# Kernel optimization log

Hardware: AMD Instinct MI355X
Metric: run time of the kernel (lower is better)

The kernel has to match this reference:

```python
import jax, jax.numpy as jnp
import numpy as np

D = 1024
H = 16

def setup_inputs() -> dict:
    key = jax.random.key(0)
    k1, k2, k3 = jax.random.split(key, 3)
    B, T = 4, 2048
    x = jax.random.normal(k1, (B, T, D), dtype=jnp.float32)
    # Linear weights stored as [in, out] so y = x @ W (equivalent to torch Linear with weight.T)
    W_attn = jax.random.normal(k2, (D, 3 * D), dtype=jnp.float32) * (1.0 / np.sqrt(D))
    W_proj = jax.random.normal(k3, (D, D), dtype=jnp.float32) * (1.0 / np.sqrt(D))
    return {"x": x, "W_attn": W_attn, "W_proj": W_proj}

def reference(x, W_attn, W_proj):
    B, T, _ = x.shape
    hd = D // H  # head dim
    qkv = x @ W_attn  # [B,T,3D]
    q, k, v = jnp.split(qkv, 3, axis=-1)
    # [B,T,D] -> [B,H,T,hd]
    q = q.reshape(B, T, H, hd).transpose(0, 2, 1, 3)
    k = k.reshape(B, T, H, hd).transpose(0, 2, 1, 3)
    v = v.reshape(B, T, H, hd).transpose(0, 2, 1, 3)
    scale = 1.0 / np.sqrt(hd).astype(np.float32)
    att = jnp.einsum('bhqd,bhkd->bhqk', q, k) * scale  # [B,H,T,T]
    causal = jnp.tril(jnp.ones((T, T), dtype=bool))
    att = jnp.where(causal[None, None], att, jnp.finfo(att.dtype).min)
    att = jax.nn.softmax(att, axis=-1)
    y = jnp.einsum('bhqk,bhkd->bhqd', att, v)  # [B,H,T,hd]
    y = y.transpose(0, 2, 1, 3).reshape(B, T, D)
    return y @ W_proj
```

## Files before the change

kernel.cpp:

```cpp
#include <hip/hip_runtime.h>


typedef __bf16 bf16;
typedef __attribute__((ext_vector_type(8))) __bf16 bf16x8;
typedef __attribute__((ext_vector_type(4))) __bf16 bf16x4;
typedef __attribute__((ext_vector_type(4))) float f4;

#define BK 32

__device__ __forceinline__ void stage16(const bf16* g, bf16* l) {
    __builtin_amdgcn_global_load_lds((const __attribute__((address_space(1))) void*)g,
                                     (__attribute__((address_space(3))) void*)l,
                                     16, 0, 0);
}

__global__ __launch_bounds__(256)
void cast_f32_bf16(const float* __restrict__ src, bf16* __restrict__ dst, int n4)
{
    int i = blockIdx.x * 256 + threadIdx.x;
    if (i < n4) {
        float4 v = ((const float4*)src)[i];
        bf16x4 o = { (bf16)v.x, (bf16)v.y, (bf16)v.z, (bf16)v.w };
        *(bf16x4*)&dst[i * 4] = o;
    }
}

__global__ __launch_bounds__(256)
void transpose_f32_bf16(const float* __restrict__ src, bf16* __restrict__ dst,
                        int R, int C)
{
    __shared__ bf16 tile[64][65];
    int c0 = blockIdx.x * 64, r0 = blockIdx.y * 64;
    int tid = threadIdx.x;
    for (int i = tid; i < 64 * 64; i += 256) {
        int r = i >> 6, c = i & 63;
        tile[r][c] = (bf16)src[(long)(r0 + r) * C + c0 + c];
    }
    __syncthreads();
    for (int i = tid; i < 64 * 64; i += 256) {
        int r = i >> 6, c = i & 63;
        dst[(long)(c0 + r) * R + r0 + c] = tile[c][r];
    }
}

template <typename OutT>
__global__ __launch_bounds__(256)
void gemm_bt(const bf16* __restrict__ A, const bf16* __restrict__ Bt,
             OutT* __restrict__ C, int M, int N, int K, int lda, int ldc)
{
    __shared__ bf16 As[128 * BK];
    __shared__ bf16 Bs[128 * BK];
    int tid = threadIdx.x;
    int lane = tid & 63;
    int wid = tid >> 6;
    int wy = wid >> 1, wx = wid & 1;

    int nwg = gridDim.x * gridDim.y;
    int bid = blockIdx.y * gridDim.x + blockIdx.x;
    int swz = (bid & 7) * (nwg >> 3) + (bid >> 3);
    int bx = swz % gridDim.x, by = swz / gridDim.x;
    int m0 = by * 128, n0 = bx * 128;

    f4 acc[4][4];
    #pragma unroll
    for (int mi = 0; mi < 4; ++mi)
        #pragma unroll
        for (int ni = 0; ni < 4; ++ni)
            acc[mi][ni] = (f4){0.f, 0.f, 0.f, 0.f};

    int srow = lane >> 2;
    int scol = (lane & 3) * 8;
    for (int kt = 0; kt < K; kt += BK) {
        #pragma unroll
        for (int i = 0; i < 2; ++i) {
            int chunk = wid * 2 + i;
            int row = chunk * 16 + srow;
            stage16(A  + (long)(m0 + row) * lda + kt + scol, As + chunk * 512 + lane * 8);
            stage16(Bt + (long)(n0 + row) * K   + kt + scol, Bs + chunk * 512 + lane * 8);
        }
        __syncthreads();
        bf16x8 af[4], bfr[4];
        #pragma unroll
        for (int mi = 0; mi < 4; ++mi)
            af[mi] = *(const bf16x8*)&As[(wy * 64 + mi * 16 + (lane & 15)) * BK + (lane >> 4) * 8];
        #pragma unroll
        for (int ni = 0; ni < 4; ++ni)
            bfr[ni] = *(const bf16x8*)&Bs[(wx * 64 + ni * 16 + (lane & 15)) * BK + (lane >> 4) * 8];
        #pragma unroll
        for (int mi = 0; mi < 4; ++mi)
            #pragma unroll
            for (int ni = 0; ni < 4; ++ni)
                acc[mi][ni] = __builtin_amdgcn_mfma_f32_16x16x32_bf16(af[mi], bfr[ni], acc[mi][ni], 0, 0, 0);
        __syncthreads();
    }
    #pragma unroll
    for (int mi = 0; mi < 4; ++mi) {
        int rbase = m0 + wy * 64 + mi * 16 + (lane >> 4) * 4;
        #pragma unroll
        for (int ni = 0; ni < 4; ++ni) {
            int col = n0 + wx * 64 + ni * 16 + (lane & 15);
            #pragma unroll
            for (int r = 0; r < 4; ++r)
                C[(long)(rbase + r) * ldc + col] = (OutT)acc[mi][ni][r];
        }
    }
}

#define QS 72
#define C_SL 0.18033688011112042f

__device__ __forceinline__ int vsw(int d, int k) {
    return d * 64 + ((((k >> 3) ^ (d & 7) ^ ((d >> 3) & 7)) & 7) << 3) + (k & 7);
}

__global__ __launch_bounds__(256)
void attn_mfma(bf16* __restrict__ qkv)
{
    __shared__ bf16 Ks[64 * QS];
    __shared__ bf16 Vt[64 * 64];
    __shared__ bf16 Ps[4 * 32 * QS];
    const int T = 2048, D3 = 3072;
    int tid = threadIdx.x;
    int lane = tid & 63, wid = tid >> 6;
    int quad = lane >> 4, col = lane & 15;
    int bh = blockIdx.x & 63;
    int g = blockIdx.x >> 6;
    int qt = ((g >> 2) & 1) ? ((g + 4) & 15) : (15 - g);
    int b = bh >> 4, h = bh & 15;
    long base = (long)b * T * D3 + h * 64;
    int q0 = qt * 128;
    int nk = 2 * qt + 2;
    int srow = tid >> 2, dseg = (tid & 3) * 16;
    bf16* Pw = &Ps[wid * 32 * QS];

    bf16x8 aq[2][2];
    #pragma unroll
    for (int nt = 0; nt < 2; ++nt) {
        const bf16* gq = &qkv[base + (long)(q0 + wid * 32 + nt * 16 + col) * D3 + quad * 8];
        aq[nt][0] = *(const bf16x8*)gq;
        aq[nt][1] = *(const bf16x8*)(gq + 32);
    }
    bf16 one1 = (bf16)1.0f;
    bf16x8 bones = {one1, one1, one1, one1, one1, one1, one1, one1};

    f4 of[2][4], lac[2];
    #pragma unroll
    for (int mg = 0; mg < 2; ++mg) {
        lac[mg] = (f4){0.f, 0.f, 0.f, 0.f};
        #pragma unroll
        for (int n = 0; n < 4; ++n) of[mg][n] = (f4){0.f, 0.f, 0.f, 0.f};
    }

    const bf16* g0 = &qkv[base + (long)srow * D3 + 1024 + dseg];
    bf16x8 kr0 = *(const bf16x8*)g0;
    bf16x8 kr1 = *(const bf16x8*)(g0 + 8);
    bf16x8 vr0 = *(const bf16x8*)(g0 + 1024);
    bf16x8 vr1 = *(const bf16x8*)(g0 + 1032);

    for (int kt = 0; kt < nk; ++kt) {
        __syncthreads();
        *(bf16x8*)&Ks[srow * QS + dseg]     = kr0;
        *(bf16x8*)&Ks[srow * QS + dseg + 8] = kr1;
        #pragma unroll
        for (int j = 0; j < 8; ++j) {
            Vt[vsw(dseg + j, srow)]     = vr0[j];
            Vt[vsw(dseg + 8 + j, srow)] = vr1[j];
        }
        if (kt + 1 < nk) {
            const bf16* gn = &qkv[base + (long)((kt + 1) * 64 + srow) * D3 + 1024 + dseg];
            kr0 = *(const bf16x8*)gn;
            kr1 = *(const bf16x8*)(gn + 8);
            vr0 = *(const bf16x8*)(gn + 1024);
            vr1 = *(const bf16x8*)(gn + 1032);
        }
        __syncthreads();
        bool diag = (kt >= nk - 2);
        int k0 = kt * 64;
        #pragma unroll
        for (int mt = 0; mt < 4; ++mt) {
            bf16x8 ak0 = *(const bf16x8*)&Ks[(mt * 16 + col) * QS + quad * 8];
            bf16x8 ak1 = *(const bf16x8*)&Ks[(mt * 16 + col) * QS + 32 + quad * 8];
            #pragma unroll
            for (int nt = 0; nt < 2; ++nt) {
                f4 z = (f4){0.f, 0.f, 0.f, 0.f};
                __builtin_amdgcn_s_setprio(1);
                z = __builtin_amdgcn_mfma_f32_16x16x32_bf16(ak0, aq[nt][0], z, 0, 0, 0);
                f4 st = __builtin_amdgcn_mfma_f32_16x16x32_bf16(ak1, aq[nt][1], z, 0, 0, 0);
                __builtin_amdgcn_s_setprio(0);
                bf16x4 pk;
                if (diag) {
                    int qg = q0 + wid * 32 + nt * 16 + col;
                    #pragma unroll
                    for (int r = 0; r < 4; ++r) {
                        float arg = fmaf(st[r], C_SL, -16.f);
                        if ((k0 + mt * 16 + quad * 4 + r) > qg) arg = -1e30f;
                        pk[r] = (bf16)exp2f(arg);
                    }
                } else {
                    #pragma unroll
                    for (int r = 0; r < 4; ++r)
                        pk[r] = (bf16)exp2f(fmaf(st[r], C_SL, -16.f));
                }
                *(bf16x4*)&Pw[(nt * 16 + col) * QS + mt * 16 + quad * 4] = pk;
            }
        }
        bf16x8 ap[2][2];
        #pragma unroll
        for (int mg = 0; mg < 2; ++mg) {
            ap[mg][0] = *(const bf16x8*)&Pw[(mg * 16 + col) * QS + quad * 8];
            ap[mg][1] = *(const bf16x8*)&Pw[(mg * 16 + col) * QS + 32 + quad * 8];
        }
        #pragma unroll
        for (int nd = 0; nd < 4; ++nd) {
            bf16x8 bv0 = *(const bf16x8*)&Vt[vsw(nd * 16 + col, quad * 8)];
            bf16x8 bv1 = *(const bf16x8*)&Vt[vsw(nd * 16 + col, 32 + quad * 8)];
            __builtin_amdgcn_s_setprio(1);
            of[0][nd] = __builtin_amdgcn_mfma_f32_16x16x32_bf16(ap[0][0], bv0, of[0][nd], 0, 0, 0);
            of[0][nd] = __builtin_amdgcn_mfma_f32_16x16x32_bf16(ap[0][1], bv1, of[0][nd], 0, 0, 0);
            of[1][nd] = __builtin_amdgcn_mfma_f32_16x16x32_bf16(ap[1][0], bv0, of[1][nd], 0, 0, 0);
            of[1][nd] = __builtin_amdgcn_mfma_f32_16x16x32_bf16(ap[1][1], bv1, of[1][nd], 0, 0, 0);
            __builtin_amdgcn_s_setprio(0);
        }
        __builtin_amdgcn_s_setprio(1);
        #pragma unroll
        for (int mg = 0; mg < 2; ++mg) {
            lac[mg] = __builtin_amdgcn_mfma_f32_16x16x32_bf16(ap[mg][0], bones, lac[mg], 0, 0, 0);
            lac[mg] = __builtin_amdgcn_mfma_f32_16x16x32_bf16(ap[mg][1], bones, lac[mg], 0, 0, 0);
        }
        __builtin_amdgcn_s_setprio(0);
    }
    #pragma unroll
    for (int mg = 0; mg < 2; ++mg)
        #pragma unroll
        for (int r = 0; r < 4; ++r) {
            float inv = 1.f / lac[mg][r];
            long yoff = base + (long)(q0 + wid * 32 + mg * 16 + quad * 4 + r) * D3;
            #pragma unroll
            for (int nd = 0; nd < 4; ++nd)
                qkv[yoff + nd * 16 + col] = (bf16)(of[mg][nd][r] * inv);
        }
}

extern "C" void kernel_launch(void* const* d_in, const int* in_sizes, int n_in,
                              void* d_out, int out_size, void* d_ws, size_t ws_size,
                              hipStream_t stream) {
    const float* x      = (const float*)d_in[0];
    const float* W_attn = (const float*)d_in[1];
    const float* W_proj = (const float*)d_in[2];
    float* out = (float*)d_out;

    bf16* qkv = (bf16*)d_ws;
    bf16* WtA = qkv + (size_t)8192 * 3072;
    bf16* WtP = WtA + (size_t)3072 * 1024;
    bf16* xb = (bf16*)d_out;

    cast_f32_bf16<<<8192, 256, 0, stream>>>(x, xb, 8192 * 1024 / 4);
    transpose_f32_bf16<<<dim3(48, 16), 256, 0, stream>>>(W_attn, WtA, 1024, 3072);
    transpose_f32_bf16<<<dim3(16, 16), 256, 0, stream>>>(W_proj, WtP, 1024, 1024);
    gemm_bt<bf16><<<dim3(24, 64), 256, 0, stream>>>(xb, WtA, qkv, 8192, 3072,
                                                    1024, 1024, 3072);
    attn_mfma<<<1024, 256, 0, stream>>>(qkv);
    gemm_bt<float><<<dim3(8, 64), 256, 0, stream>>>(qkv, WtP, out, 8192, 1024,
                                                    1024, 3072, 1024);
}
```

Before: 269.1 us.

## Replace QKV GEMM with 256x256-tile 8-wave pipelined kernel using async LDS loads

Adds a new GEMM kernel for the QKV projection. Each block has 512 threads and computes a 256x256 output tile. Operands are staged into 128KB of dynamic LDS with double-buffered direct global-to-LDS loads, split into quarter-chunks and interleaved with MFMA phases using vmcnt waits, barriers and setprio. The goal is more data reuse per tile and overlap of global loads with matrix math. The attention kernel's query-tile ordering is also simplified to a plain descending order, which changes load balancing across blocks.

After: 282.9 us. 5.1% more time.

```diff
diff --git a/kernel.cpp b/kernel.cpp
--- a/kernel.cpp
+++ b/kernel.cpp
@@ -106,6 +106,145 @@
     }
 }
 
+#define VM8  asm volatile("s_waitcnt vmcnt(8)" ::: "memory")
+#define CLOB asm volatile("" ::: "memory")
+#define BARR __builtin_amdgcn_s_barrier()
+
+__global__ __launch_bounds__(512)
+void gemm256(const bf16* __restrict__ A, const bf16* __restrict__ Bt,
+             bf16* __restrict__ C, int M, int N, int K, int ldc)
+{
+    extern __shared__ bf16 lds[];
+    bf16* Asl = lds;
+    bf16* Bsl = lds + 32768;
+    int tid = threadIdx.x;
+    int lane = tid & 63, wid = tid >> 6;
+    int wm = wid >> 2, wn = wid & 3;
+    int quad = lane >> 4, col = lane & 15;
+
+    int nwg = gridDim.x * gridDim.y;
+    int bid = blockIdx.y * gridDim.x + blockIdx.x;
+    int swz = (bid & 7) * (nwg >> 3) + (bid >> 3);
+    int bx = swz % gridDim.x, by = swz / gridDim.x;
+    int m0 = by * 256, n0 = bx * 256;
+
+    int NT = K >> 6;
+    int srow0 = wid * 8 + (lane >> 3);
+    int scol0 = (lane & 7) * 8;
+
+    f4 acc[8][4];
+    #pragma unroll
+    for (int mi = 0; mi < 8; ++mi)
+        #pragma unroll
+        for (int ni = 0; ni < 4; ++ni)
+            acc[mi][ni] = (f4){0.f, 0.f, 0.f, 0.f};
+
+    #define STAGE_S(sv) do {                                                   \
+        int _s = (sv);                                                         \
+        int _ts = _s >> 2; if (_ts > NT - 1) _ts = NT - 1;                     \
+        int _c = _s & 3;                                                       \
+        const bf16* _mat = (_c & 1) ? A : Bt;                                  \
+        int _hh = _c >> 1;                                                     \
+        bf16* _base = ((_c & 1) ? Asl : Bsl) + ((_ts & 1) * 2 + _hh) * 8192;   \
+        int _rb = ((_c & 1) ? m0 : n0) + _hh * 128;                            \
+        _Pragma("unroll")                                                      \
+        for (int _i = 0; _i < 2; ++_i)                                         \
+            stage16(_mat + (long)(_rb + _i * 64 + srow0) * K + _ts * 64 + scol0,\
+                    _base + (_i * 64 + srow0) * 64 + scol0);                   \
+    } while (0)
+
+    #pragma unroll
+    for (int s = 0; s < 6; ++s) STAGE_S(s);
+    int s = 6;
+
+    bf16x8 a[4][2], bb[2][2][2];
+    int aoff0 = (wm * 128 + col) * 64 + quad * 8;
+    int boff0 = ((wn >> 1) * 128 + (wn & 1) * 64 + col) * 64 + quad * 8;
+
+    for (int t = 0; t < NT; ++t) {
+        int b = t & 1;
+        int aoff = b * 16384 + aoff0;
+        int boff = b * 16384 + boff0;
+        VM8; STAGE_S(s); ++s; CLOB; BARR; CLOB;
+        #pragma unroll
+        for (int mi = 0; mi < 4; ++mi)
+            #pragma unroll
+            for (int kk = 0; kk < 2; ++kk)
+                a[mi][kk] = *(const bf16x8*)&Asl[aoff + mi * 1024 + kk * 32];
+        #pragma unroll
+        for (int ni = 0; ni < 2; ++ni)
+            #pragma unroll
+            for (int kk = 0; kk < 2; ++kk)
+                bb[0][ni][kk] = *(const bf16x8*)&Bsl[boff + ni * 1024 + kk * 32];
+        __builtin_amdgcn_s_setprio(1);
+        #pragma unroll
+        for (int mi = 0; mi < 4; ++mi)
+            #pragma unroll
+            for (int ni = 0; ni < 2; ++ni)
+                #pragma unroll
+                for (int kk = 0; kk < 2; ++kk)
+                    acc[mi][ni] = __builtin_amdgcn_mfma_f32_16x16x32_bf16(a[mi][kk], bb[0][ni][kk], acc[mi][ni], 0, 0, 0);
+        __builtin_amdgcn_s_setprio(0);
+        CLOB; BARR;
+        VM8; STAGE_S(s); ++s; CLOB; BARR; CLOB;
+        #pragma unroll
+        for (int ni = 0; ni < 2; ++ni)
+            #pragma unroll
+            for (int kk = 0; kk < 2; ++kk)
+                bb[1][ni][kk] = *(const bf16x8*)&Bsl[boff + 2048 + ni * 1024 + kk * 32];
+        __builtin_amdgcn_s_setprio(1);
+        #pragma unroll
+        for (int mi = 0; mi < 4; ++mi)
+            #pragma unroll
+            for (int ni = 0; ni < 2; ++ni)
+                #pragma unroll
+                for (int kk = 0; kk < 2; ++kk)
+                    acc[mi][2 + ni] = __builtin_amdgcn_mfma_f32_16x16x32_bf16(a[mi][kk], bb[1][ni][kk], acc[mi][2 + ni], 0, 0, 0);
+        __builtin_amdgcn_s_setprio(0);
+        CLOB; BARR;
+        VM8; STAGE_S(s); ++s; CLOB; BARR; CLOB;
+        #pragma unroll
+        for (int mi = 0; mi < 4; ++mi)
+            #pragma unroll
+            for (int kk = 0; kk < 2; ++kk)
+                a[mi][kk] = *(const bf16x8*)&Asl[aoff + 4096 + mi * 1024 + kk * 32];
+        __builtin_amdgcn_s_setprio(1);
+        #pragma unroll
+        for (int mi = 0; mi < 4; ++mi)
+            #pragma unroll
+            for (int ni = 0; ni < 2; ++ni)
+                #pragma unroll
+                for (int kk = 0; kk < 2; ++kk)
+                    acc[4 + mi][2 + ni] = __builtin_amdgcn_mfma_f32_16x16x32_bf16(a[mi][kk], bb[1][ni][kk], acc[4 + mi][2 + ni], 0, 0, 0);
+        __builtin_amdgcn_s_setprio(0);
+        CLOB; BARR;
+        STAGE_S(s); ++s; CLOB; BARR; CLOB;
+        __builtin_amdgcn_s_setprio(1);
+        #pragma unroll
+        for (int mi = 0; mi < 4; ++mi)
+            #pragma unroll
+            for (int ni = 0; ni < 2; ++ni)
+                #pragma unroll
+                for (int kk = 0; kk < 2; ++kk)
+                    acc[4 + mi][ni] = __builtin_amdgcn_mfma_f32_16x16x32_bf16(a[mi][kk], bb[0][ni][kk], acc[4 + mi][ni], 0, 0, 0);
+        __builtin_amdgcn_s_setprio(0);
+        CLOB; BARR;
+    }
+    #undef STAGE_S
+
+    #pragma unroll
+    for (int mi = 0; mi < 8; ++mi) {
+        int rbase = m0 + wm * 128 + mi * 16 + quad * 4;
+        #pragma unroll
+        for (int ni = 0; ni < 4; ++ni) {
+            int cc = n0 + wn * 64 + ni * 16 + col;
+            #pragma unroll
+            for (int r = 0; r < 4; ++r)
+                C[(long)(rbase + r) * ldc + cc] = (bf16)acc[mi][ni][r];
+        }
+    }
+}
+
 #define QS 72
 #define C_SL 0.18033688011112042f
 
@@ -124,8 +263,7 @@
     int lane = tid & 63, wid = tid >> 6;
     int quad = lane >> 4, col = lane & 15;
     int bh = blockIdx.x & 63;
-    int g = blockIdx.x >> 6;
-    int qt = ((g >> 2) & 1) ? ((g + 4) & 15) : (15 - g);
+    int qt = 15 - (blockIdx.x >> 6);
     int b = bh >> 4, h = bh & 15;
     long base = (long)b * T * D3 + h * 64;
     int q0 = qt * 128;
@@ -254,11 +392,18 @@
     bf16* WtP = WtA + (size_t)3072 * 1024;
     bf16* xb = (bf16*)d_out;
 
+    static bool attr_set = false;
+    if (!attr_set) {
+        hipFuncSetAttribute((const void*)gemm256,
+                            hipFuncAttributeMaxDynamicSharedMemorySize, 131072);
+        attr_set = true;
+    }
+
     cast_f32_bf16<<<8192, 256, 0, stream>>>(x, xb, 8192 * 1024 / 4);
     transpose_f32_bf16<<<dim3(48, 16), 256, 0, stream>>>(W_attn, WtA, 1024, 3072);
     transpose_f32_bf16<<<dim3(16, 16), 256, 0, stream>>>(W_proj, WtP, 1024, 1024);
-    gemm_bt<bf16><<<dim3(24, 64), 256, 0, stream>>>(xb, WtA, qkv, 8192, 3072,
-                                                    1024, 1024, 3072);
+    gemm256<<<dim3(12, 32), 512, 131072, stream>>>(xb, WtA, qkv, 8192, 3072,
+                                                   1024, 3072);
     attn_mfma<<<1024, 256, 0, stream>>>(qkv);
     gemm_bt<float><<<dim3(8, 64), 256, 0, stream>>>(qkv, WtP, out, 8192, 1024,
                                                     1024, 3072, 1024);
```

## Add 256x256-tile pipelined GEMM for QKV projection with swizzled LDS

Applied to the files above, without the earlier changes.

Replaces the QKV projection GEMM with a new 512-thread kernel that uses 256x256 output tiles, a BK of 64, double-buffered direct-to-LDS loads with XOR-swizzled layout, and barrier-interleaved MFMA phases with priority hints. A grid-block swizzle groups workgroups for L2 locality. It is meant to raise arithmetic intensity and overlap global loads with MFMA work. The attention kernel's q-tile ordering is also simplified to a plain descending order. The GEMM needs 128KB of dynamic LDS, so each CU holds only one workgroup and the grid has fewer, larger blocks.

Result: no change. 265.2 us (-1.4%).

```diff
diff --git a/kernel.cpp b/kernel.cpp
--- a/kernel.cpp
+++ b/kernel.cpp
@@ -102,6 +102,120 @@
             #pragma unroll
             for (int r = 0; r < 4; ++r)
                 C[(long)(rbase + r) * ldc + col] = (OutT)acc[mi][ni][r];
+        }
+    }
+}
+
+#define VMW8 asm volatile("s_waitcnt vmcnt(8)" ::: "memory")
+#define VMW0 asm volatile("s_waitcnt vmcnt(0)" ::: "memory")
+#define CLOB asm volatile("" ::: "memory")
+#define BARR __builtin_amdgcn_s_barrier()
+#define SB0  __builtin_amdgcn_sched_barrier(0)
+
+__global__ __launch_bounds__(512)
+void gemm256(const bf16* __restrict__ A, const bf16* __restrict__ Bt,
+             bf16* __restrict__ C, int M, int N, int K, int ldc)
+{
+    extern __shared__ bf16 lds[];
+    bf16* Asl = lds;
+    bf16* Bsl = lds + 32768;
+    int tid = threadIdx.x;
+    int lane = tid & 63, wid = tid >> 6;
+    int wm = wid >> 2, wn = wid & 3;
+    int quad = lane >> 4, col = lane & 15;
+
+    int nwg = gridDim.x * gridDim.y;
+    int bid = blockIdx.y * gridDim.x + blockIdx.x;
+    int swz = (bid & 7) * (nwg >> 3) + (bid >> 3);
+    int bx = swz % gridDim.x, by = swz / gridDim.x;
+    int m0 = by * 256, n0 = bx * 256;
+
+    int NT = K >> 6;
+    int srow = wid * 8 + (lane >> 3);
+    int lincol = (lane & 7) * 8;
+    int swcol  = ((lane & 7) ^ ((lane >> 3) & 7)) * 8;
+    int xorv = (col & 7) << 4;
+    int ke0 = ((quad * 16) ^ xorv) >> 1;
+    int ke1 = ((quad * 16 + 64) ^ xorv) >> 1;
+
+    f4 acc[8][4];
+    #pragma unroll
+    for (int mi = 0; mi < 8; ++mi)
+        #pragma unroll
+        for (int ni = 0; ni < 4; ++ni)
+            acc[mi][ni] = (f4){0.f, 0.f, 0.f, 0.f};
+
+    #define STG_HALF(mat, rb, ts, dstb) do {                                    \
+        _Pragma("unroll")                                                       \
+        for (int _i = 0; _i < 2; ++_i)                                          \
+            stage16((mat) + (long)((rb) + _i * 64 + srow) * K + (ts) * 64 + swcol, \
+                    (dstb) + (_i * 64 + srow) * 64 + lincol);                   \
+    } while (0)
+    #define STGB(ts) do { bf16* _d = Bsl + ((ts) & 1) * 16384;                  \
+        STG_HALF(Bt, n0,       (ts), _d);                                       \
+        STG_HALF(Bt, n0 + 128, (ts), _d + 8192); } while (0)
+    #define STGA(ts) do { bf16* _d = Asl + ((ts) & 1) * 16384;                  \
+        STG_HALF(A,  m0,       (ts), _d);                                       \
+        STG_HALF(A,  m0 + 128, (ts), _d + 8192); } while (0)
+
+    bf16x8 a[4][2], bb[2][2][2];
+    #define RD_A(qm) do { _Pragma("unroll")                                     \
+        for (int mi = 0; mi < 4; ++mi) {                                        \
+            int _r = ab + ((qm) * 64 + mi * 16) * 64;                           \
+            a[mi][0] = *(const bf16x8*)&Asl[_r + ke0];                          \
+            a[mi][1] = *(const bf16x8*)&Asl[_r + ke1]; } } while (0)
+    #define RD_B(qn) do { _Pragma("unroll")                                     \
+        for (int ni = 0; ni < 2; ++ni) {                                        \
+            int _r = bbo + ((qn) * 32 + ni * 16) * 64;                          \
+            bb[qn][ni][0] = *(const bf16x8*)&Bsl[_r + ke0];                     \
+            bb[qn][ni][1] = *(const bf16x8*)&Bsl[_r + ke1]; } } while (0)
+    #define MM(qm, qn) do { __builtin_amdgcn_s_setprio(1);                      \
+        _Pragma("unroll")                                                       \
+        for (int mi = 0; mi < 4; ++mi)                                          \
+            _Pragma("unroll")                                                   \
+            for (int ni = 0; ni < 2; ++ni)                                      \
+                _Pragma("unroll")                                               \
+                for (int kk = 0; kk < 2; ++kk)                                  \
+                    acc[(qm)*4+mi][(qn)*2+ni] =                                 \
+                        __builtin_amdgcn_mfma_f32_16x16x32_bf16(                \
+                            a[mi][kk], bb[qn][ni][kk],                          \
+                            acc[(qm)*4+mi][(qn)*2+ni], 0, 0, 0);                \
+        __builtin_amdgcn_s_setprio(0); } while (0)
+
+    STGB(0); STGA(0); STGB(1); STGA(1);
+    VMW8; CLOB; BARR; CLOB;
+
+    for (int t = 0; t < NT; ++t) {
+        int b = t & 1;
+        int ab  = b * 16384 + (wm * 128 + col) * 64;
+        int bbo = b * 16384 + (wn * 64 + col) * 64;
+        RD_A(0); RD_B(0);
+        CLOB; BARR; SB0; MM(0, 0); CLOB; BARR;
+        RD_B(1);
+        CLOB; BARR; SB0; MM(0, 1); CLOB; BARR;
+        RD_A(1);
+        if (t + 2 < NT) STGB(t + 2);
+        CLOB; BARR; SB0; MM(1, 1); CLOB; BARR;
+        if (t + 2 < NT) { STGA(t + 2); VMW8; }
+        else if (t + 1 < NT) { VMW0; }
+        CLOB; BARR; SB0; MM(1, 0); CLOB; BARR;
+    }
+    #undef STG_HALF
+    #undef STGB
+    #undef STGA
+    #undef RD_A
+    #undef RD_B
+    #undef MM
+
+    #pragma unroll
+    for (int mi = 0; mi < 8; ++mi) {
+        int rbase = m0 + wm * 128 + mi * 16 + quad * 4;
+        #pragma unroll
+        for (int ni = 0; ni < 4; ++ni) {
+            int cc = n0 + wn * 64 + ni * 16 + col;
+            #pragma unroll
+            for (int r = 0; r < 4; ++r)
+                C[(long)(rbase + r) * ldc + cc] = (bf16)acc[mi][ni][r];
         }
     }
 }
@@ -124,8 +238,7 @@
     int lane = tid & 63, wid = tid >> 6;
     int quad = lane >> 4, col = lane & 15;
     int bh = blockIdx.x & 63;
-    int g = blockIdx.x >> 6;
-    int qt = ((g >> 2) & 1) ? ((g + 4) & 15) : (15 - g);
+    int qt = 15 - (blockIdx.x >> 6);
     int b = bh >> 4, h = bh & 15;
     long base = (long)b * T * D3 + h * 64;
     int q0 = qt * 128;
@@ -254,11 +367,18 @@
     bf16* WtP = WtA + (size_t)3072 * 1024;
     bf16* xb = (bf16*)d_out;
 
+    static bool attr_set = false;
+    if (!attr_set) {
+        hipFuncSetAttribute((const void*)gemm256,
+                            hipFuncAttributeMaxDynamicSharedMemorySize, 131072);
+        attr_set = true;
+    }
+
     cast_f32_bf16<<<8192, 256, 0, stream>>>(x, xb, 8192 * 1024 / 4);
     transpose_f32_bf16<<<dim3(48, 16), 256, 0, stream>>>(W_attn, WtA, 1024, 3072);
     transpose_f32_bf16<<<dim3(16, 16), 256, 0, stream>>>(W_proj, WtP, 1024, 1024);
-    gemm_bt<bf16><<<dim3(24, 64), 256, 0, stream>>>(xb, WtA, qkv, 8192, 3072,
-                                                    1024, 1024, 3072);
+    gemm256<<<dim3(12, 32), 512, 131072, stream>>>(xb, WtA, qkv, 8192, 3072,
+                                                   1024, 3072);
     attn_mfma<<<1024, 256, 0, stream>>>(qkv);
     gemm_bt<float><<<dim3(8, 64), 256, 0, stream>>>(qkv, WtP, out, 8192, 1024,
                                                     1024, 3072, 1024);
```

## Replace GEMM with 128x256-tile double-buffered pipelined 512-thread kernel

Applied to the files above, without the earlier changes.

Replaces the simple 128x128 GEMM with a 512-thread kernel using 128x256 tiles and BK=64. It double-buffers LDS through direct global-to-LDS loads with an XOR-swizzled layout and interleaves MFMA phases with prefetch and explicit vmcnt waits and barriers. The goal is to hide global-memory latency, cut LDS bank conflicts and raise the MFMA share of runtime for both projection GEMMs. The attention kernel's query-tile ordering is also simplified to a plain descending order. The cost is 96KB of dynamic LDS per block, which lowers occupancy, and a more fragile synchronisation scheme.

New measurement: 255.6 us. 5.0% less time.

```diff
diff --git a/kernel.cpp b/kernel.cpp
--- a/kernel.cpp
+++ b/kernel.cpp
@@ -5,8 +5,6 @@
 typedef __attribute__((ext_vector_type(8))) __bf16 bf16x8;
 typedef __attribute__((ext_vector_type(4))) __bf16 bf16x4;
 typedef __attribute__((ext_vector_type(4))) float f4;
-
-#define BK 32
 
 __device__ __forceinline__ void stage16(const bf16* g, bf16* l) {
     __builtin_amdgcn_global_load_lds((const __attribute__((address_space(1))) void*)g,
@@ -43,23 +41,38 @@
     }
 }
 
+#define VMW6 asm volatile("s_waitcnt vmcnt(6)" ::: "memory")
+#define VMW0 asm volatile("s_waitcnt vmcnt(0)" ::: "memory")
+#define CLOB asm volatile("" ::: "memory")
+#define BARR __builtin_amdgcn_s_barrier()
+#define SB0  __builtin_amdgcn_sched_barrier(0)
+
 template <typename OutT>
-__global__ __launch_bounds__(256)
-void gemm_bt(const bf16* __restrict__ A, const bf16* __restrict__ Bt,
-             OutT* __restrict__ C, int M, int N, int K, int lda, int ldc)
+__global__ __launch_bounds__(512)
+void gemm256(const bf16* __restrict__ A, const bf16* __restrict__ Bt,
+             OutT* __restrict__ C, int lda, int ldb, int ldc, int K)
 {
-    __shared__ bf16 As[128 * BK];
-    __shared__ bf16 Bs[128 * BK];
+    extern __shared__ bf16 lds[];
+    bf16* Asl = lds;
+    bf16* Bsl = lds + 16384;
     int tid = threadIdx.x;
-    int lane = tid & 63;
-    int wid = tid >> 6;
-    int wy = wid >> 1, wx = wid & 1;
+    int lane = tid & 63, wid = tid >> 6;
+    int wm = wid >> 2, wn = wid & 3;
+    int quad = lane >> 4, col = lane & 15;
 
     int nwg = gridDim.x * gridDim.y;
     int bid = blockIdx.y * gridDim.x + blockIdx.x;
     int swz = (bid & 7) * (nwg >> 3) + (bid >> 3);
     int bx = swz % gridDim.x, by = swz / gridDim.x;
-    int m0 = by * 128, n0 = bx * 128;
+    int m0 = by * 128, n0 = bx * 256;
+
+    int NT = K >> 6;
+    int srow = wid * 8 + (lane >> 3);
+    int lincol = (lane & 7) * 8;
+    int swcol  = ((lane & 7) ^ ((lane >> 3) & 7)) * 8;
+    int xorv = (col & 7) << 4;
+    int ke0 = ((quad * 16) ^ xorv) >> 1;
+    int ke1 = ((quad * 16 + 64) ^ xorv) >> 1;
 
     f4 acc[4][4];
     #pragma unroll
@@ -68,40 +81,75 @@
         for (int ni = 0; ni < 4; ++ni)
             acc[mi][ni] = (f4){0.f, 0.f, 0.f, 0.f};
 
-    int srow = lane >> 2;
-    int scol = (lane & 3) * 8;
-    for (int kt = 0; kt < K; kt += BK) {
-        #pragma unroll
-        for (int i = 0; i < 2; ++i) {
-            int chunk = wid * 2 + i;
-            int row = chunk * 16 + srow;
-            stage16(A  + (long)(m0 + row) * lda + kt + scol, As + chunk * 512 + lane * 8);
-            stage16(Bt + (long)(n0 + row) * K   + kt + scol, Bs + chunk * 512 + lane * 8);
-        }
-        __syncthreads();
-        bf16x8 af[4], bfr[4];
-        #pragma unroll
-        for (int mi = 0; mi < 4; ++mi)
-            af[mi] = *(const bf16x8*)&As[(wy * 64 + mi * 16 + (lane & 15)) * BK + (lane >> 4) * 8];
-        #pragma unroll
-        for (int ni = 0; ni < 4; ++ni)
-            bfr[ni] = *(const bf16x8*)&Bs[(wx * 64 + ni * 16 + (lane & 15)) * BK + (lane >> 4) * 8];
-        #pragma unroll
-        for (int mi = 0; mi < 4; ++mi)
-            #pragma unroll
-            for (int ni = 0; ni < 4; ++ni)
-                acc[mi][ni] = __builtin_amdgcn_mfma_f32_16x16x32_bf16(af[mi], bfr[ni], acc[mi][ni], 0, 0, 0);
-        __syncthreads();
-    }
+    #define STG_HALF(mat, rb, ld, ts, dstb) do {                                \
+        _Pragma("unroll")                                                       \
+        for (int _i = 0; _i < 2; ++_i)                                          \
+            stage16((mat) + (long)((rb) + _i * 64 + srow) * (ld) + (ts) * 64 + swcol, \
+                    (dstb) + (_i * 64 + srow) * 64 + lincol);                   \
+    } while (0)
+    #define STGA(ts) STG_HALF(A, m0, lda, (ts), Asl + ((ts) & 1) * 8192)
+    #define STGB(ts) do { bf16* _d = Bsl + ((ts) & 1) * 16384;                  \
+        STG_HALF(Bt, n0,       ldb, (ts), _d);                                  \
+        STG_HALF(Bt, n0 + 128, ldb, (ts), _d + 8192); } while (0)
+
+    bf16x8 a[2][2], bb[4][2];
+    #define RD_A(mp) do { _Pragma("unroll")                                     \
+        for (int _m = 0; _m < 2; ++_m) {                                        \
+            int _r = ab + ((mp) * 2 + _m) * 1024;                               \
+            a[_m][0] = *(const bf16x8*)&Asl[_r + ke0];                          \
+            a[_m][1] = *(const bf16x8*)&Asl[_r + ke1]; } } while (0)
+    #define RD_B(np) do { _Pragma("unroll")                                     \
+        for (int _n = 0; _n < 2; ++_n) {                                        \
+            int _r = bbo + ((np) * 2 + _n) * 1024;                              \
+            bb[(np)*2+_n][0] = *(const bf16x8*)&Bsl[_r + ke0];                  \
+            bb[(np)*2+_n][1] = *(const bf16x8*)&Bsl[_r + ke1]; } } while (0)
+    #define MM(mp, np) do { __builtin_amdgcn_s_setprio(1);                      \
+        _Pragma("unroll")                                                       \
+        for (int _m = 0; _m < 2; ++_m)                                          \
+            _Pragma("unroll")                                                   \
+            for (int _n = 0; _n < 2; ++_n)                                      \
+                _Pragma("unroll")                                               \
+                for (int kk = 0; kk < 2; ++kk)                                  \
+                    acc[(mp)*2+_m][(np)*2+_n] =                                 \
+                        __builtin_amdgcn_mfma_f32_16x16x32_bf16(                \
+                            a[_m][kk], bb[(np)*2+_n][kk],                       \
+                            acc[(mp)*2+_m][(np)*2+_n], 0, 0, 0);                \
+        __builtin_amdgcn_s_setprio(0); } while (0)
+
+    STGB(0); STGA(0); STGB(1); STGA(1);
+    VMW6; CLOB; BARR; CLOB;
+
+    for (int t = 0; t < NT; ++t) {
+        int b = t & 1;
+        int ab  = b * 8192  + (wm * 64 + col) * 64;
+        int bbo = b * 16384 + (wn * 64 + col) * 64;
+        RD_A(0); RD_B(0);
+        CLOB; BARR; SB0; MM(0, 0); CLOB; BARR;
+        RD_B(1);
+        CLOB; BARR; SB0; MM(0, 1); CLOB; BARR;
+        RD_A(1);
+        if (t + 2 < NT) STGB(t + 2);
+        CLOB; BARR; SB0; MM(1, 1); CLOB; BARR;
+        if (t + 2 < NT) { STGA(t + 2); VMW6; }
+        else if (t + 1 < NT) { VMW0; }
+        CLOB; BARR; SB0; MM(1, 0); CLOB; BARR;
+    }
+    #undef STG_HALF
+    #undef STGA
+    #undef STGB
+    #undef RD_A
+    #undef RD_B
+    #undef MM
+
     #pragma unroll
     for (int mi = 0; mi < 4; ++mi) {
-        int rbase = m0 + wy * 64 + mi * 16 + (lane >> 4) * 4;
+        int rbase = m0 + wm * 64 + mi * 16 + quad * 4;
         #pragma unroll
         for (int ni = 0; ni < 4; ++ni) {
-            int col = n0 + wx * 64 + ni * 16 + (lane & 15);
+            int cc = n0 + wn * 64 + ni * 16 + col;
             #pragma unroll
             for (int r = 0; r < 4; ++r)
-                C[(long)(rbase + r) * ldc + col] = (OutT)acc[mi][ni][r];
+                C[(long)(rbase + r) * ldc + cc] = (OutT)acc[mi][ni][r];
         }
     }
 }
@@ -124,8 +172,7 @@
     int lane = tid & 63, wid = tid >> 6;
     int quad = lane >> 4, col = lane & 15;
     int bh = blockIdx.x & 63;
-    int g = blockIdx.x >> 6;
-    int qt = ((g >> 2) & 1) ? ((g + 4) & 15) : (15 - g);
+    int qt = 15 - (blockIdx.x >> 6);
     int b = bh >> 4, h = bh & 15;
     long base = (long)b * T * D3 + h * 64;
     int q0 = qt * 128;
@@ -254,12 +301,21 @@
     bf16* WtP = WtA + (size_t)3072 * 1024;
     bf16* xb = (bf16*)d_out;
 
+    static bool attr_set = false;
+    if (!attr_set) {
+        hipFuncSetAttribute((const void*)gemm256<bf16>,
+                            hipFuncAttributeMaxDynamicSharedMemorySize, 98304);
+        hipFuncSetAttribute((const void*)gemm256<float>,
+                            hipFuncAttributeMaxDynamicSharedMemorySize, 98304);
+        attr_set = true;
+    }
+
     cast_f32_bf16<<<8192, 256, 0, stream>>>(x, xb, 8192 * 1024 / 4);
     transpose_f32_bf16<<<dim3(48, 16), 256, 0, stream>>>(W_attn, WtA, 1024, 3072);
     transpose_f32_bf16<<<dim3(16, 16), 256, 0, stream>>>(W_proj, WtP, 1024, 1024);
-    gemm_bt<bf16><<<dim3(24, 64), 256, 0, stream>>>(xb, WtA, qkv, 8192, 3072,
-                                                    1024, 1024, 3072);
+    gemm256<bf16><<<dim3(12, 64), 512, 98304, stream>>>(xb, WtA, qkv,
+                                                        1024, 1024, 3072, 1024);
     attn_mfma<<<1024, 256, 0, stream>>>(qkv);
-    gemm_bt<float><<<dim3(8, 64), 256, 0, stream>>>(qkv, WtP, out, 8192, 1024,
-                                                    1024, 3072, 1024);
-}
+    gemm256<float><<<dim3(4, 64), 512, 98304, stream>>>(qkv, WtP, out,
+                                                        3072, 1024, 1024, 1024);
+}
```
